# Kernel optimization log

Hardware: AMD Instinct MI355X
Metric: run time of the kernel (lower is better)

Reference implementation:

```python
import jax, jax.numpy as jnp
import numpy as np

N_NODES = 50000
N_REL = 20
EMB = 64
HID = 128
N_EDGES = 1600000
BATCH = 8192


def _rgcn_layer(x, src, dst, etype, W, root, b):
    # PyG RGCNConv with aggr='mean', no basis decomposition:
    # out[i] = sum_r W_r @ mean_{j in N_r(i)} x[j] + root @ x[i] + b
    # Mean commutes with the linear map, so aggregate x[src] per (dst, rel)
    # first, then apply W_r once per relation.
    n, r = N_NODES, N_REL
    seg = dst * r + etype                                   # [E]
    msg = x[src]                                            # [E, d_in]
    agg = jax.ops.segment_sum(msg, seg, num_segments=n * r)  # [N*R, d_in]
    cnt = jax.ops.segment_sum(jnp.ones(src.shape, x.dtype), seg, num_segments=n * r)
    mean = agg / jnp.maximum(cnt, 1.0)[:, None]
    mean = mean.reshape(n, r, -1)                           # [N, R, d_in]
    return jnp.einsum('nri,rio->no', mean, W) + x @ root + b


def setup_inputs() -> dict:
    key = jax.random.key(0)
    ks = jax.random.split(key, 16)
    edge_index = jax.random.randint(ks[0], (2, N_EDGES), 0, N_NODES, dtype=jnp.int64 if jax.config.jax_enable_x64 else jnp.int32)
    edge_type = jax.random.randint(ks[1], (N_EDGES,), 0, N_REL)
    head_indices = jax.random.randint(ks[2], (BATCH,), 0, N_NODES)
    tail_indices = jax.random.randint(ks[3], (BATCH,), 0, N_NODES)
    relation_types = jax.random.randint(ks[4], (BATCH,), 0, N_REL)

    def xavier(k, shape):
        fan_in, fan_out = shape[-2], shape[-1]
        lim = float(np.sqrt(6.0 / (fan_in + fan_out)))
        return jax.random.uniform(k, shape, jnp.float32, -lim, lim)

    node_emb = xavier(ks[5], (N_NODES, EMB))
    W1 = xavier(ks[6], (N_REL, EMB, HID))
    root1 = xavier(ks[7], (EMB, HID))
    b1 = jnp.zeros((HID,), jnp.float32)
    W2 = xavier(ks[8], (N_REL, HID, HID))
    root2 = xavier(ks[9], (HID, HID))
    b2 = jnp.zeros((HID,), jnp.float32)
    rel_emb = xavier(ks[10], (N_REL, HID))
    return dict(edge_index=edge_index, edge_type=edge_type,
                head_indices=head_indices, tail_indices=tail_indices,
                relation_types=relation_types, node_emb=node_emb,
                W1=W1, root1=root1, b1=b1, W2=W2, root2=root2, b2=b2,
                rel_emb=rel_emb)


def reference(edge_index, edge_type, head_indices, tail_indices, relation_types,
              node_emb, W1, root1, b1, W2, root2, b2, rel_emb):
    src, dst = edge_index[0], edge_index[1]
    # RGCN encoder (eval mode: dropout is identity)
    h = _rgcn_layer(node_emb, src, dst, edge_type, W1, root1, b1)
    h = jax.nn.relu(h)
    h = _rgcn_layer(h, src, dst, edge_type, W2, root2, b2)
    # DistMult decoder
    head = h[head_indices]
    tail = h[tail_indices]
    r = rel_emb[relation_types]
    scores = jnp.sum(head * r * tail, axis=1)               # [B]
    return scores
```

## Files before the change

### kernel.cpp

```cpp
#include <hip/hip_runtime.h>
#include <hip/hip_bf16.h>

#define NNODES 50000
#define NREL   20
#define NSEG   (NNODES * NREL)
#define DEMB   64
#define DHID   128

typedef __attribute__((ext_vector_type(8))) short short8;
typedef __attribute__((ext_vector_type(4))) float f32x4;

__device__ __forceinline__ unsigned short bf16rn(float x) {
    unsigned u = __builtin_bit_cast(unsigned, x);
    unsigned r = u + 0x7FFFu + ((u >> 16) & 1u);
    return (unsigned short)(r >> 16);
}
__device__ __forceinline__ float bf16tof(unsigned short h) {
    return __builtin_bit_cast(float, (unsigned)h << 16);
}


__global__ void hist_kernel(const int* __restrict__ dst, const int* __restrict__ et,
                            int E, int* __restrict__ cnt) {
    for (int e = blockIdx.x * blockDim.x + threadIdx.x; e < E; e += gridDim.x * blockDim.x) {
        atomicAdd(&cnt[dst[e] * NREL + et[e]], 1);
    }
}

__global__ void scan_partial(const int* __restrict__ cnt, int* __restrict__ bsum, int n) {
    __shared__ int s[256];
    int base = blockIdx.x * 1024;
    int t = threadIdx.x;
    int v = 0;
    for (int i = t; i < 1024; i += 256) {
        int idx = base + i;
        v += (idx < n) ? cnt[idx] : 0;
    }
    s[t] = v;
    __syncthreads();
    for (int o = 128; o > 0; o >>= 1) {
        if (t < o) s[t] += s[t + o];
        __syncthreads();
    }
    if (t == 0) bsum[blockIdx.x] = s[0];
}

__global__ void scan_bsums(int* __restrict__ bsum, int nb) {
    __shared__ int s[1024];
    int t = threadIdx.x;
    s[t] = (t < nb) ? bsum[t] : 0;
    __syncthreads();
    for (int o = 1; o < 1024; o <<= 1) {
        int v = (t >= o) ? s[t - o] : 0;
        __syncthreads();
        s[t] += v;
        __syncthreads();
    }
    if (t < nb) bsum[t] = (t == 0) ? 0 : s[t - 1];
}

__global__ void scan_final(const int* __restrict__ cnt, const int* __restrict__ bsum,
                           int* __restrict__ off, int n) {
    __shared__ int s[256];
    int base = blockIdx.x * 1024;
    int t = threadIdx.x;
    int idx = base + t * 4;
    int a0 = (idx + 0 < n) ? cnt[idx + 0] : 0;
    int a1 = (idx + 1 < n) ? cnt[idx + 1] : 0;
    int a2 = (idx + 2 < n) ? cnt[idx + 2] : 0;
    int a3 = (idx + 3 < n) ? cnt[idx + 3] : 0;
    s[t] = a0 + a1 + a2 + a3;
    __syncthreads();
    for (int o = 1; o < 256; o <<= 1) {
        int v = (t >= o) ? s[t - o] : 0;
        __syncthreads();
        s[t] += v;
        __syncthreads();
    }
    int base_ex = ((t == 0) ? 0 : s[t - 1]) + bsum[blockIdx.x];
    if (idx + 0 < n) off[idx + 0] = base_ex;
    if (idx + 1 < n) off[idx + 1] = base_ex + a0;
    if (idx + 2 < n) off[idx + 2] = base_ex + a0 + a1;
    if (idx + 3 < n) off[idx + 3] = base_ex + a0 + a1 + a2;
}

__global__ void place_kernel(const int* __restrict__ src, const int* __restrict__ dst,
                             const int* __restrict__ et, int E,
                             int* __restrict__ off_mut, int* __restrict__ csr_src) {
    for (int e = blockIdx.x * blockDim.x + threadIdx.x; e < E; e += gridDim.x * blockDim.x) {
        int seg = dst[e] * NREL + et[e];
        int p = atomicAdd(&off_mut[seg], 1);
        csr_src[p] = src[e];
    }
}

template <int K>
__global__ void prep_w(const float* __restrict__ W, const float* __restrict__ root,
                       short* __restrict__ Wt) {
    constexpr int KS = K / 32;
    int idx = blockIdx.x * blockDim.x + threadIdx.x;
    int total = (NREL + 1) * 128 * K;
    if (idx >= total) return;
    int r   = idx / (128 * K);
    int rem = idx % (128 * K);
    int c   = rem / K;
    int k   = rem % K;
    float v = (r < NREL) ? W[((size_t)r * K + k) * 128 + c] : root[(size_t)k * 128 + c];
    unsigned short hi = bf16rn(v);
    unsigned short lo = bf16rn(v - bf16tof(hi));
    int s = k >> 5, kk = k & 31;
    size_t base = ((size_t)r * KS + s) * 10240 + (size_t)c * 40 + kk;
    Wt[base]        = (short)hi;
    Wt[base + 5120] = (short)lo;
}


__device__ __forceinline__ void stage40(const short* __restrict__ gsrc,
                                        short* ldst, int t, int nbytes) {
    const int u = t >> 6, lane = t & 63;
    #pragma unroll
    for (int j = 0; j < 8; ++j) {
        int blk = u + j * 8;
        if (blk * 1024 >= nbytes) break;
        __builtin_amdgcn_global_load_lds(
            (const __attribute__((address_space(1))) void*)((const char*)gsrc + blk * 1024 + lane * 16),
            (__attribute__((address_space(3))) void*)((char*)ldst + blk * 1024 + lane * 16),
            16, 0, 0);
    }
}

template <int K, bool RELU>
__global__ __launch_bounds__(512, 4) void rgcn_layer_kernel(
    const float* __restrict__ X,
    const short* __restrict__ Wt,
    const float* __restrict__ bias,
    const int* __restrict__ off,
    const int* __restrict__ cnt,
    const int* __restrict__ csr_src,
    float* __restrict__ H,
    int nnodes)
{
    constexpr int NB  = 128;
    constexpr int NQ  = K / 32;
    constexpr int NPH = K / 64;
    constexpr int RSs = 72;
    constexpr int PS  = NB * RSs;

    __shared__ short meanS[2 * PS];
    __shared__ short Wbuf[20480];

    const int n0 = blockIdx.x * NB;
    const int t  = threadIdx.x;
    const int l  = t & 63;
    const int w  = t >> 6;
    const int rg = w & 3;
    const int cg = w >> 2;
    const int q8 = (l >> 4) * 8;

    const int team  = t >> 3;
    const int lane8 = t & 7;

    f32x4 acc[2][4];
    #pragma unroll
    for (int ct = 0; ct < 4; ++ct) {
        const float b = bias[cg * 64 + ct * 16 + (l & 15)];
        #pragma unroll
        for (int rt = 0; rt < 2; ++rt) acc[rt][ct] = (f32x4){b, b, b, b};
    }

    for (int rr = 0; rr <= NREL; ++rr) {
        __syncthreads();

        const short* wtRel = Wt + (size_t)rr * (2 * NPH) * 10240;

        stage40(wtRel, Wbuf, t, 40960);

        const int nA = n0 + team;
        const int nB = n0 + team + 64;
        float sAx[NQ], sAy[NQ], sAz[NQ], sAw[NQ];
        float sBx[NQ], sBy[NQ], sBz[NQ], sBw[NQ];
        #pragma unroll
        for (int q = 0; q < NQ; ++q) {
            sAx[q] = sAy[q] = sAz[q] = sAw[q] = 0.f;
            sBx[q] = sBy[q] = sBz[q] = sBw[q] = 0.f;
        }
        float invA = 1.0f, invB = 1.0f;

        if (rr < NREL) {
            int cA = 0, oA = 0, cB = 0, oB = 0;
            if (nA < nnodes) { const int sg = nA * NREL + rr; cA = cnt[sg]; oA = off[sg] - cA; }
            if (nB < nnodes) { const int sg = nB * NREL + rr; cB = cnt[sg]; oB = off[sg] - cB; }
            const int jmax = max(cA, cB);
            for (int j = 0; j < jmax; ++j) {
                const bool pa = j < cA, pb = j < cB;
                const int ia = csr_src[pa ? (oA + j) : 0];
                const int ib = csr_src[pb ? (oB + j) : 0];
                const float* pxA = X + (size_t)ia * K;
                const float* pxB = X + (size_t)ib * K;
                float4 vA[NQ], vB[NQ];
                #pragma unroll
                for (int q = 0; q < NQ; ++q) vA[q] = *(const float4*)&pxA[q * 32 + lane8 * 4];
                #pragma unroll
                for (int q = 0; q < NQ; ++q) vB[q] = *(const float4*)&pxB[q * 32 + lane8 * 4];
                if (pa) {
                    #pragma unroll
                    for (int q = 0; q < NQ; ++q) {
                        sAx[q] += vA[q].x; sAy[q] += vA[q].y; sAz[q] += vA[q].z; sAw[q] += vA[q].w;
                    }
                }
                if (pb) {
                    #pragma unroll
                    for (int q = 0; q < NQ; ++q) {
                        sBx[q] += vB[q].x; sBy[q] += vB[q].y; sBz[q] += vB[q].z; sBw[q] += vB[q].w;
                    }
                }
            }
            invA = 1.0f / (float)max(cA, 1);
            invB = 1.0f / (float)max(cB, 1);
        } else {
            if (nA < nnodes) {
                const float* xr = X + (size_t)nA * K;
                #pragma unroll
                for (int q = 0; q < NQ; ++q) {
                    const float4 v = *(const float4*)&xr[q * 32 + lane8 * 4];
                    sAx[q] = v.x; sAy[q] = v.y; sAz[q] = v.z; sAw[q] = v.w;
                }
            }
            if (nB < nnodes) {
                const float* xr = X + (size_t)nB * K;
                #pragma unroll
                for (int q = 0; q < NQ; ++q) {
                    const float4 v = *(const float4*)&xr[q * 32 + lane8 * 4];
                    sBx[q] = v.x; sBy[q] = v.y; sBz[q] = v.z; sBw[q] = v.w;
                }
            }
        }
        #pragma unroll
        for (int q = 0; q < NQ; ++q) {
            sAx[q] *= invA; sAy[q] *= invA; sAz[q] *= invA; sAw[q] *= invA;
            sBx[q] *= invB; sBy[q] *= invB; sBz[q] *= invB; sBw[q] *= invB;
        }

        #pragma unroll
        for (int p = 0; p < NPH; ++p) {
            if (p == 1) {
                __syncthreads();
                stage40(wtRel + 2 * 10240, Wbuf, t, 40960);
            }
            #pragma unroll
            for (int qq = 0; qq < 2; ++qq) {
                const int qg = p * 2 + qq;
                const int kb = qq * 32 + lane8 * 4;
                {
                    const float vx = sAx[qg], vy = sAy[qg], vz = sAz[qg], vw = sAw[qg];
                    const unsigned short hx = bf16rn(vx), hy = bf16rn(vy), hz = bf16rn(vz), hw = bf16rn(vw);
                    short4 hi4, lo4;
                    hi4.x = (short)hx; hi4.y = (short)hy; hi4.z = (short)hz; hi4.w = (short)hw;
                    lo4.x = (short)bf16rn(vx - bf16tof(hx));
                    lo4.y = (short)bf16rn(vy - bf16tof(hy));
                    lo4.z = (short)bf16rn(vz - bf16tof(hz));
                    lo4.w = (short)bf16rn(vw - bf16tof(hw));
                    *(short4*)&meanS[team * RSs + kb]      = hi4;
                    *(short4*)&meanS[PS + team * RSs + kb] = lo4;
                }
                {
                    const float vx = sBx[qg], vy = sBy[qg], vz = sBz[qg], vw = sBw[qg];
                    const unsigned short hx = bf16rn(vx), hy = bf16rn(vy), hz = bf16rn(vz), hw = bf16rn(vw);
                    short4 hi4, lo4;
                    hi4.x = (short)hx; hi4.y = (short)hy; hi4.z = (short)hz; hi4.w = (short)hw;
                    lo4.x = (short)bf16rn(vx - bf16tof(hx));
                    lo4.y = (short)bf16rn(vy - bf16tof(hy));
                    lo4.z = (short)bf16rn(vz - bf16tof(hz));
                    lo4.w = (short)bf16rn(vw - bf16tof(hw));
                    *(short4*)&meanS[(team + 64) * RSs + kb]      = hi4;
                    *(short4*)&meanS[PS + (team + 64) * RSs + kb] = lo4;
                }
            }

            __syncthreads();

            #pragma unroll
            for (int ls = 0; ls < 2; ++ls) {
                short8 bf[4][2];
                #pragma unroll
                for (int ct = 0; ct < 4; ++ct) {
                    const int col = cg * 64 + ct * 16 + (l & 15);
                    bf[ct][0] = *(const short8*)&Wbuf[ls * 10240 +        col * 40 + q8];
                    bf[ct][1] = *(const short8*)&Wbuf[ls * 10240 + 5120 + col * 40 + q8];
                }
                #pragma unroll
                for (int rt = 0; rt < 2; ++rt) {
                    const int row = rg * 32 + rt * 16 + (l & 15);
                    const int ka  = row * RSs + ls * 32 + q8;
                    const short8 a0 = *(const short8*)&meanS[ka];
                    const short8 a1 = *(const short8*)&meanS[PS + ka];
                    #pragma unroll
                    for (int ct = 0; ct < 4; ++ct) {
                        acc[rt][ct] = __builtin_amdgcn_mfma_f32_16x16x32_bf16(a0, bf[ct][0], acc[rt][ct], 0, 0, 0);
                        acc[rt][ct] = __builtin_amdgcn_mfma_f32_16x16x32_bf16(a0, bf[ct][1], acc[rt][ct], 0, 0, 0);
                        acc[rt][ct] = __builtin_amdgcn_mfma_f32_16x16x32_bf16(a1, bf[ct][0], acc[rt][ct], 0, 0, 0);
                    }
                }
            }
        }
    }

    #pragma unroll
    for (int rt = 0; rt < 2; ++rt) {
        #pragma unroll
        for (int reg = 0; reg < 4; ++reg) {
            const int node = n0 + rg * 32 + rt * 16 + (l >> 4) * 4 + reg;
            if (node < nnodes) {
                #pragma unroll
                for (int ct = 0; ct < 4; ++ct) {
                    float v = acc[rt][ct][reg];
                    if (RELU) v = fmaxf(v, 0.0f);
                    H[(size_t)node * 128 + cg * 64 + ct * 16 + (l & 15)] = v;
                }
            }
        }
    }
}

__global__ void decoder_kernel(const float* __restrict__ H, const float* __restrict__ rel_emb,
                               const int* __restrict__ head, const int* __restrict__ tail,
                               const int* __restrict__ rt, float* __restrict__ out, int B) {
    const int idx  = blockIdx.x * blockDim.x + threadIdx.x;
    const int b    = idx >> 6;
    const int lane = idx & 63;
    if (b >= B) return;
    const float* hp = H + (size_t)head[b] * 128;
    const float* tp = H + (size_t)tail[b] * 128;
    const float* rp = rel_emb + (size_t)rt[b] * 128;
    double s = 0.0;
    #pragma unroll
    for (int c = 0; c < 2; ++c) {
        const int k = lane + c * 64;
        s += (double)hp[k] * (double)rp[k] * (double)tp[k];
    }
    for (int o = 32; o > 0; o >>= 1) s += __shfl_down(s, o);
    if (lane == 0) out[b] = (float)s;
}


extern "C" void kernel_launch(void* const* d_in, const int* in_sizes, int n_in,
                              void* d_out, int out_size, void* d_ws, size_t ws_size,
                              hipStream_t stream) {
    const int*   edge_index = (const int*)d_in[0];
    const int*   edge_type  = (const int*)d_in[1];
    const int*   head       = (const int*)d_in[2];
    const int*   tail       = (const int*)d_in[3];
    const int*   rtyp       = (const int*)d_in[4];
    const float* node_emb   = (const float*)d_in[5];
    const float* W1         = (const float*)d_in[6];
    const float* root1      = (const float*)d_in[7];
    const float* b1         = (const float*)d_in[8];
    const float* W2         = (const float*)d_in[9];
    const float* root2      = (const float*)d_in[10];
    const float* b2         = (const float*)d_in[11];
    const float* rel_emb    = (const float*)d_in[12];
    float* out = (float*)d_out;

    const int E = in_sizes[1];
    const int B = in_sizes[2];
    const int* src = edge_index;
    const int* dst = edge_index + E;

    char* ws = (char*)d_ws;
    size_t o = 0;
    auto carve = [&](size_t bytes) { char* p = ws + o; o += (bytes + 255) & ~size_t(255); return p; };
    int*   off     = (int*)carve(sizeof(int) * NSEG);
    int*   cnt     = (int*)carve(sizeof(int) * NSEG);
    int*   csr_src = (int*)carve(sizeof(int) * (size_t)E);
    int*   bsum    = (int*)carve(sizeof(int) * 1024);
    float* h1      = (float*)carve(sizeof(float) * (size_t)NNODES * DHID);
    float* h2      = (float*)carve(sizeof(float) * (size_t)NNODES * DHID);
    short* Wt1     = (short*)carve(sizeof(short) * (size_t)(NREL + 1) * 2 * 10240);
    short* Wt2     = (short*)carve(sizeof(short) * (size_t)(NREL + 1) * 4 * 10240);
    (void)ws_size;

    const int NCHUNK = (NSEG + 1023) / 1024;

    {
        const int tot1 = (NREL + 1) * 128 * DEMB;
        const int tot2 = (NREL + 1) * 128 * DHID;
        prep_w<DEMB><<<(tot1 + 255) / 256, 256, 0, stream>>>(W1, root1, Wt1);
        prep_w<DHID><<<(tot2 + 255) / 256, 256, 0, stream>>>(W2, root2, Wt2);
    }

    hipMemsetAsync(cnt, 0, sizeof(int) * NSEG, stream);
    hist_kernel<<<2048, 256, 0, stream>>>(dst, edge_type, E, cnt);
    scan_partial<<<NCHUNK, 256, 0, stream>>>(cnt, bsum, NSEG);
    scan_bsums<<<1, 1024, 0, stream>>>(bsum, NCHUNK);
    scan_final<<<NCHUNK, 256, 0, stream>>>(cnt, bsum, off, NSEG);
    place_kernel<<<2048, 256, 0, stream>>>(src, dst, edge_type, E, off, csr_src);

    const int LBLK = (NNODES + 127) / 128;
    rgcn_layer_kernel<DEMB, true ><<<LBLK, 512, 0, stream>>>(node_emb, Wt1, b1,
                                                             off, cnt, csr_src, h1, NNODES);
    rgcn_layer_kernel<DHID, false><<<LBLK, 512, 0, stream>>>(h1, Wt2, b2,
                                                             off, cnt, csr_src, h2, NNODES);

    decoder_kernel<<<(B * 64 + 255) / 256, 256, 0, stream>>>(h2, rel_emb, head, tail, rtyp, out, B);
}
```

Measured before the change: 732.0 us.

## Split relation loop across two grid halves with atomic accumulation and deferred ReLU

Each RGCN layer now launches a 2D grid in which blockIdx.y picks half of the relations (0-10 or 11-20, the last being the root). The two halves add their partial results into pre-zeroed outputs with float atomics. Because the output is now only partial until both halves finish, the ReLU moves from the first layer's store to the second layer's input loads. The weight staging buffer shrinks to one K=32 slice at a time, cutting LDS use, which may allow more resident blocks. This doubles the number of blocks to raise occupancy on the gather-bound loop, at the cost of two memsets, atomic traffic and results that depend on summation order.

Result: slower. 762.3 us (+4.1%).

```diff
diff --git a/kernel.cpp b/kernel.cpp
--- a/kernel.cpp
+++ b/kernel.cpp
@@ -115,13 +115,13 @@
 }
 
 
-__device__ __forceinline__ void stage40(const short* __restrict__ gsrc,
-                                        short* ldst, int t, int nbytes) {
+__device__ __forceinline__ void stage20(const short* __restrict__ gsrc,
+                                        short* ldst, int t) {
     const int u = t >> 6, lane = t & 63;
     #pragma unroll
-    for (int j = 0; j < 8; ++j) {
+    for (int j = 0; j < 3; ++j) {
         int blk = u + j * 8;
-        if (blk * 1024 >= nbytes) break;
+        if (blk >= 20) break;
         __builtin_amdgcn_global_load_lds(
             (const __attribute__((address_space(1))) void*)((const char*)gsrc + blk * 1024 + lane * 16),
             (__attribute__((address_space(3))) void*)((char*)ldst + blk * 1024 + lane * 16),
@@ -129,7 +129,7 @@
     }
 }
 
-template <int K, bool RELU>
+template <int K, bool RELU_IN>
 __global__ __launch_bounds__(512, 4) void rgcn_layer_kernel(
     const float* __restrict__ X,
     const short* __restrict__ Wt,
@@ -142,14 +142,15 @@
 {
     constexpr int NB  = 128;
     constexpr int NQ  = K / 32;
-    constexpr int NPH = K / 64;
-    constexpr int RSs = 72;
-    constexpr int PS  = NB * RSs;
-
-    __shared__ short meanS[2 * PS];
-    __shared__ short Wbuf[20480];
+    constexpr int KS  = K / 32;
+    constexpr int QSs = 40;
+    constexpr int PSq = NB * QSs;
+
+    __shared__ short meanS[2 * PSq];
+    __shared__ short Wbuf[10240];
 
     const int n0 = blockIdx.x * NB;
+    const int ry = blockIdx.y;
     const int t  = threadIdx.x;
     const int l  = t & 63;
     const int w  = t >> 6;
@@ -163,17 +164,19 @@
     f32x4 acc[2][4];
     #pragma unroll
     for (int ct = 0; ct < 4; ++ct) {
-        const float b = bias[cg * 64 + ct * 16 + (l & 15)];
+        const float b = (ry == 0) ? bias[cg * 64 + ct * 16 + (l & 15)] : 0.0f;
         #pragma unroll
         for (int rt = 0; rt < 2; ++rt) acc[rt][ct] = (f32x4){b, b, b, b};
     }
 
-    for (int rr = 0; rr <= NREL; ++rr) {
-        __syncthreads();
-
-        const short* wtRel = Wt + (size_t)rr * (2 * NPH) * 10240;
-
-        stage40(wtRel, Wbuf, t, 40960);
+    const int r0 = ry ? 11 : 0;
+    const int r1 = ry ? 21 : 11;
+
+    for (int rr = r0; rr < r1; ++rr) {
+        __syncthreads();
+
+        const short* wtRel = Wt + (size_t)rr * KS * 10240;
+        stage20(wtRel, Wbuf, t);
 
         const int nA = n0 + team;
         const int nB = n0 + team + 64;
@@ -184,7 +187,6 @@
             sAx[q] = sAy[q] = sAz[q] = sAw[q] = 0.f;
             sBx[q] = sBy[q] = sBz[q] = sBw[q] = 0.f;
         }
-        float invA = 1.0f, invB = 1.0f;
 
         if (rr < NREL) {
             int cA = 0, oA = 0, cB = 0, oB = 0;
@@ -202,6 +204,15 @@
                 for (int q = 0; q < NQ; ++q) vA[q] = *(const float4*)&pxA[q * 32 + lane8 * 4];
                 #pragma unroll
                 for (int q = 0; q < NQ; ++q) vB[q] = *(const float4*)&pxB[q * 32 + lane8 * 4];
+                if (RELU_IN) {
+                    #pragma unroll
+                    for (int q = 0; q < NQ; ++q) {
+                        vA[q].x = fmaxf(vA[q].x, 0.f); vA[q].y = fmaxf(vA[q].y, 0.f);
+                        vA[q].z = fmaxf(vA[q].z, 0.f); vA[q].w = fmaxf(vA[q].w, 0.f);
+                        vB[q].x = fmaxf(vB[q].x, 0.f); vB[q].y = fmaxf(vB[q].y, 0.f);
+                        vB[q].z = fmaxf(vB[q].z, 0.f); vB[q].w = fmaxf(vB[q].w, 0.f);
+                    }
+                }
                 if (pa) {
                     #pragma unroll
                     for (int q = 0; q < NQ; ++q) {
@@ -215,14 +226,21 @@
                     }
                 }
             }
-            invA = 1.0f / (float)max(cA, 1);
-            invB = 1.0f / (float)max(cB, 1);
+            const float invA = 1.0f / (float)max(cA, 1);
+            const float invB = 1.0f / (float)max(cB, 1);
+            #pragma unroll
+            for (int q = 0; q < NQ; ++q) {
+                sAx[q] *= invA; sAy[q] *= invA; sAz[q] *= invA; sAw[q] *= invA;
+                sBx[q] *= invB; sBy[q] *= invB; sBz[q] *= invB; sBw[q] *= invB;
+            }
         } else {
             if (nA < nnodes) {
                 const float* xr = X + (size_t)nA * K;
                 #pragma unroll
                 for (int q = 0; q < NQ; ++q) {
-                    const float4 v = *(const float4*)&xr[q * 32 + lane8 * 4];
+                    float4 v = *(const float4*)&xr[q * 32 + lane8 * 4];
+                    if (RELU_IN) { v.x = fmaxf(v.x, 0.f); v.y = fmaxf(v.y, 0.f);
+                                   v.z = fmaxf(v.z, 0.f); v.w = fmaxf(v.w, 0.f); }
                     sAx[q] = v.x; sAy[q] = v.y; sAz[q] = v.z; sAw[q] = v.w;
                 }
             }
@@ -230,29 +248,24 @@
                 const float* xr = X + (size_t)nB * K;
                 #pragma unroll
                 for (int q = 0; q < NQ; ++q) {
-                    const float4 v = *(const float4*)&xr[q * 32 + lane8 * 4];
+                    float4 v = *(const float4*)&xr[q * 32 + lane8 * 4];
+                    if (RELU_IN) { v.x = fmaxf(v.x, 0.f); v.y = fmaxf(v.y, 0.f);
+                                   v.z = fmaxf(v.z, 0.f); v.w = fmaxf(v.w, 0.f); }
                     sBx[q] = v.x; sBy[q] = v.y; sBz[q] = v.z; sBw[q] = v.w;
                 }
             }
         }
+
         #pragma unroll
-        for (int q = 0; q < NQ; ++q) {
-            sAx[q] *= invA; sAy[q] *= invA; sAz[q] *= invA; sAw[q] *= invA;
-            sBx[q] *= invB; sBy[q] *= invB; sBz[q] *= invB; sBw[q] *= invB;
-        }
-
-        #pragma unroll
-        for (int p = 0; p < NPH; ++p) {
-            if (p == 1) {
+        for (int q = 0; q < KS; ++q) {
+            if (q > 0) {
                 __syncthreads();
-                stage40(wtRel + 2 * 10240, Wbuf, t, 40960);
-            }
-            #pragma unroll
-            for (int qq = 0; qq < 2; ++qq) {
-                const int qg = p * 2 + qq;
-                const int kb = qq * 32 + lane8 * 4;
+                stage20(wtRel + q * 10240, Wbuf, t);
+            }
+            {
+                const int kb = lane8 * 4;
                 {
-                    const float vx = sAx[qg], vy = sAy[qg], vz = sAz[qg], vw = sAw[qg];
+                    const float vx = sAx[q], vy = sAy[q], vz = sAz[q], vw = sAw[q];
                     const unsigned short hx = bf16rn(vx), hy = bf16rn(vy), hz = bf16rn(vz), hw = bf16rn(vw);
                     short4 hi4, lo4;
                     hi4.x = (short)hx; hi4.y = (short)hy; hi4.z = (short)hz; hi4.w = (short)hw;
@@ -260,11 +273,11 @@
                     lo4.y = (short)bf16rn(vy - bf16tof(hy));
                     lo4.z = (short)bf16rn(vz - bf16tof(hz));
                     lo4.w = (short)bf16rn(vw - bf16tof(hw));
-                    *(short4*)&meanS[team * RSs + kb]      = hi4;
-                    *(short4*)&meanS[PS + team * RSs + kb] = lo4;
+                    *(short4*)&meanS[team * QSs + kb]       = hi4;
+                    *(short4*)&meanS[PSq + team * QSs + kb] = lo4;
                 }
                 {
-                    const float vx = sBx[qg], vy = sBy[qg], vz = sBz[qg], vw = sBw[qg];
+                    const float vx = sBx[q], vy = sBy[q], vz = sBz[q], vw = sBw[q];
                     const unsigned short hx = bf16rn(vx), hy = bf16rn(vy), hz = bf16rn(vz), hw = bf16rn(vw);
                     short4 hi4, lo4;
                     hi4.x = (short)hx; hi4.y = (short)hy; hi4.z = (short)hz; hi4.w = (short)hw;
@@ -272,34 +285,31 @@
                     lo4.y = (short)bf16rn(vy - bf16tof(hy));
                     lo4.z = (short)bf16rn(vz - bf16tof(hz));
                     lo4.w = (short)bf16rn(vw - bf16tof(hw));
-                    *(short4*)&meanS[(team + 64) * RSs + kb]      = hi4;
-                    *(short4*)&meanS[PS + (team + 64) * RSs + kb] = lo4;
-                }
-            }
-
+                    *(short4*)&meanS[(team + 64) * QSs + kb]       = hi4;
+                    *(short4*)&meanS[PSq + (team + 64) * QSs + kb] = lo4;
+                }
+            }
             __syncthreads();
 
+            short8 bhi[4], blo[4];
             #pragma unroll
-            for (int ls = 0; ls < 2; ++ls) {
-                short8 bf[4][2];
+            for (int ct = 0; ct < 4; ++ct) {
+                const int col = cg * 64 + ct * 16 + (l & 15);
+                bhi[ct] = *(const short8*)&Wbuf[       col * 40 + q8];
+                blo[ct] = *(const short8*)&Wbuf[5120 + col * 40 + q8];
+            }
+
+            #pragma unroll
+            for (int rt = 0; rt < 2; ++rt) {
+                const int row = rg * 32 + rt * 16 + (l & 15);
+                const int ka  = row * QSs + q8;
+                const short8 a0 = *(const short8*)&meanS[ka];
+                const short8 a1 = *(const short8*)&meanS[PSq + ka];
                 #pragma unroll
                 for (int ct = 0; ct < 4; ++ct) {
-                    const int col = cg * 64 + ct * 16 + (l & 15);
-                    bf[ct][0] = *(const short8*)&Wbuf[ls * 10240 +        col * 40 + q8];
-                    bf[ct][1] = *(const short8*)&Wbuf[ls * 10240 + 5120 + col * 40 + q8];
-                }
-                #pragma unroll
-                for (int rt = 0; rt < 2; ++rt) {
-                    const int row = rg * 32 + rt * 16 + (l & 15);
-                    const int ka  = row * RSs + ls * 32 + q8;
-                    const short8 a0 = *(const short8*)&meanS[ka];
-                    const short8 a1 = *(const short8*)&meanS[PS + ka];
-                    #pragma unroll
-                    for (int ct = 0; ct < 4; ++ct) {
-                        acc[rt][ct] = __builtin_amdgcn_mfma_f32_16x16x32_bf16(a0, bf[ct][0], acc[rt][ct], 0, 0, 0);
-                        acc[rt][ct] = __builtin_amdgcn_mfma_f32_16x16x32_bf16(a0, bf[ct][1], acc[rt][ct], 0, 0, 0);
-                        acc[rt][ct] = __builtin_amdgcn_mfma_f32_16x16x32_bf16(a1, bf[ct][0], acc[rt][ct], 0, 0, 0);
-                    }
+                    acc[rt][ct] = __builtin_amdgcn_mfma_f32_16x16x32_bf16(a0, bhi[ct], acc[rt][ct], 0, 0, 0);
+                    acc[rt][ct] = __builtin_amdgcn_mfma_f32_16x16x32_bf16(a0, blo[ct], acc[rt][ct], 0, 0, 0);
+                    acc[rt][ct] = __builtin_amdgcn_mfma_f32_16x16x32_bf16(a1, bhi[ct], acc[rt][ct], 0, 0, 0);
                 }
             }
         }
@@ -313,9 +323,8 @@
             if (node < nnodes) {
                 #pragma unroll
                 for (int ct = 0; ct < 4; ++ct) {
-                    float v = acc[rt][ct][reg];
-                    if (RELU) v = fmaxf(v, 0.0f);
-                    H[(size_t)node * 128 + cg * 64 + ct * 16 + (l & 15)] = v;
+                    atomicAdd(&H[(size_t)node * 128 + cg * 64 + ct * 16 + (l & 15)],
+                              acc[rt][ct][reg]);
                 }
             }
         }
@@ -395,11 +404,14 @@
     scan_final<<<NCHUNK, 256, 0, stream>>>(cnt, bsum, off, NSEG);
     place_kernel<<<2048, 256, 0, stream>>>(src, dst, edge_type, E, off, csr_src);
 
-    const int LBLK = (NNODES + 127) / 128;
-    rgcn_layer_kernel<DEMB, true ><<<LBLK, 512, 0, stream>>>(node_emb, Wt1, b1,
-                                                             off, cnt, csr_src, h1, NNODES);
-    rgcn_layer_kernel<DHID, false><<<LBLK, 512, 0, stream>>>(h1, Wt2, b2,
-                                                             off, cnt, csr_src, h2, NNODES);
+    hipMemsetAsync(h1, 0, sizeof(float) * (size_t)NNODES * DHID, stream);
+    hipMemsetAsync(h2, 0, sizeof(float) * (size_t)NNODES * DHID, stream);
+
+    const dim3 LGRID((NNODES + 127) / 128, 2);
+    rgcn_layer_kernel<DEMB, false><<<LGRID, 512, 0, stream>>>(node_emb, Wt1, b1,
+                                                              off, cnt, csr_src, h1, NNODES);
+    rgcn_layer_kernel<DHID, true ><<<LGRID, 512, 0, stream>>>(h1, Wt2, b2,
+                                                              off, cnt, csr_src, h2, NNODES);
 
     decoder_kernel<<<(B * 64 + 255) / 256, 256, 0, stream>>>(h2, rel_emb, head, tail, rtyp, out, B);
 }
```
